# Kernel tuning notes

Measured on AMD Instinct MI355X. Metric: run time of the kernel, lower is better.

The kernel has to match this reference:

```python
import jax, jax.numpy as jnp
import numpy as np

N_NODES = 100000
N_EDGES = 1600000


def _glorot(key, shape):
    lim = float(np.sqrt(6.0 / (shape[0] + shape[1])))
    return jax.random.uniform(key, shape, jnp.float32, -lim, lim)


def setup_inputs() -> dict:
    key = jax.random.key(0)
    ks = jax.random.split(key, 12)
    x = jax.random.normal(ks[0], (N_NODES, 8), jnp.float32)
    edge_index = jax.random.randint(ks[1], (2, N_EDGES), 0, N_NODES, jnp.int64)
    dims = [(8, 32), (32, 32), (32, 32), (32, 32), (32, 3)]
    params = {}
    for i, (din, dout) in enumerate(dims):
        params[f"W{i+1}"] = _glorot(ks[2 + i], (din, dout))
        params[f"b{i+1}"] = jnp.zeros((dout,), jnp.float32)
    return {"x": x, "edge_index": edge_index, **params}


def _gcn_norm(edge_index, num_nodes):
    # add self-loops, symmetric normalization (PyG GCNConv defaults)
    loops = jnp.arange(num_nodes, dtype=edge_index.dtype)
    row = jnp.concatenate([edge_index[0], loops])
    col = jnp.concatenate([edge_index[1], loops])
    deg = jax.ops.segment_sum(jnp.ones_like(col, jnp.float32), col,
                              num_segments=num_nodes)
    dinv = jnp.where(deg > 0, jax.lax.rsqrt(deg), 0.0)
    norm = dinv[row] * dinv[col]  # [E + N]
    return row, col, norm


def _gcn_conv(h, W, b, row, col, norm, num_nodes):
    h = h @ W                                   # [N, dout]
    msg = h[row] * norm[:, None]                # gather + scale
    out = jax.ops.segment_sum(msg, col, num_segments=num_nodes)
    return out + b


def reference(x, edge_index, W1, b1, W2, b2, W3, b3, W4, b4, W5, b5):
    row, col, norm = _gcn_norm(edge_index, N_NODES)
    lrelu = lambda h: jax.nn.leaky_relu(h, negative_slope=1.0)  # identity, kept faithful
    h = lrelu(_gcn_conv(x, W1, b1, row, col, norm, N_NODES))
    h = lrelu(_gcn_conv(h, W2, b2, row, col, norm, N_NODES))
    h = lrelu(_gcn_conv(h, W3, b3, row, col, norm, N_NODES))
    h = lrelu(_gcn_conv(h, W4, b4, row, col, norm, N_NODES))
    h = lrelu(_gcn_conv(h, W5, b5, row, col, norm, N_NODES))
    return h
```

## Files before the change

### kernel.cpp

```cpp
#include <hip/hip_runtime.h>
#include <hip/hip_bf16.h>

#define NN 100000
#define NE 1600000
#define NB 391
#define EPB 3125
#define NBLK 512
#define CAP 4608



__global__ __launch_bounds__(256) void prep_kernel(
    const unsigned int* __restrict__ ew, int* __restrict__ is64,
    const float* __restrict__ W1, const float* __restrict__ b1,
    const float* __restrict__ W2, const float* __restrict__ b2,
    const float* __restrict__ W3, const float* __restrict__ b3,
    const float* __restrict__ W4, const float* __restrict__ b4,
    const float* __restrict__ W5, const float* __restrict__ b5,
    float* __restrict__ Wt, float* __restrict__ cv,
    int* __restrict__ bcursor) {
    __shared__ int nz;
    __shared__ float w45[32 * 3], w345[32 * 3], w2345[32 * 3];
    int tid = threadIdx.x;
    if (tid == 0) nz = 0;
    __syncthreads();
    if (ew[2 * tid + 1] != 0) atomicAdd(&nz, 1);
    for (int i = tid; i < NB; i += 256) bcursor[i] = i * CAP;
    int i = tid / 3, j = tid - 3 * (tid / 3);
    if (tid < 96) {
        float s = 0.0f;
        for (int k = 0; k < 32; k++) s += W4[i * 32 + k] * W5[k * 3 + j];
        w45[i * 3 + j] = s;
    }
    __syncthreads();
    if (tid < 96) {
        float s = 0.0f;
        for (int k = 0; k < 32; k++) s += W3[i * 32 + k] * w45[k * 3 + j];
        w345[i * 3 + j] = s;
    }
    __syncthreads();
    if (tid < 96) {
        float s = 0.0f;
        for (int k = 0; k < 32; k++) s += W2[i * 32 + k] * w345[k * 3 + j];
        w2345[i * 3 + j] = s;
    }
    __syncthreads();
    if (tid < 32) {
        int ii = tid >> 2, jj = tid & 3;
        float s = 0.0f;
        if (jj < 3)
            for (int k = 0; k < 32; k++) s += W1[ii * 32 + k] * w2345[k * 3 + jj];
        Wt[tid] = s;
    }
    if (tid >= 32 && tid < 52) {
        int kk = (tid - 32) >> 2, jj = (tid - 32) & 3;
        float s = 0.0f;
        if (jj < 3) {
            if (kk == 0) for (int k = 0; k < 32; k++) s += b1[k] * w2345[k * 3 + jj];
            if (kk == 1) for (int k = 0; k < 32; k++) s += b2[k] * w345[k * 3 + jj];
            if (kk == 2) for (int k = 0; k < 32; k++) s += b3[k] * w45[k * 3 + jj];
            if (kk == 3) for (int k = 0; k < 32; k++) s += b4[k] * W5[k * 3 + jj];
            if (kk == 4) s = b5[jj];
        }
        cv[tid - 32] = s;
    }
    if (tid == 0) *is64 = (nz == 0) ? 1 : 0;
}


__global__ __launch_bounds__(512) void bucket_scatter_kernel(const void* __restrict__ ei,
                                                             const int* __restrict__ is64,
                                                             int* __restrict__ bcursor,
                                                             unsigned int* __restrict__ epacked) {
    __shared__ int lcount[NB];
    __shared__ int lstart[NB];
    __shared__ int lcur[NB];
    __shared__ int gbase[NB];
    __shared__ int wsum[8];
    __shared__ unsigned int slotv[EPB];
    __shared__ unsigned short slotb[EPB];
    int tid = threadIdx.x;
    for (int i = tid; i < NB; i += 512) lcount[i] = 0;
    __syncthreads();
    int f = *is64;
    int base = blockIdx.x * EPB;
    int r[7], c[7];
    r[6] = -1;
    if (f == 0) {
        const int* e32 = (const int*)ei;
#pragma unroll
        for (int k = 0; k < 6; k++) {
            int e = base + k * 512 + tid;
            r[k] = e32[e];
            c[k] = e32[NE + e];
        }
        if (tid < EPB - 6 * 512) {
            int e = base + 6 * 512 + tid;
            r[6] = e32[e];
            c[6] = e32[NE + e];
        }
    } else {
        const long long* e64 = (const long long*)ei;
#pragma unroll
        for (int k = 0; k < 6; k++) {
            int e = base + k * 512 + tid;
            r[k] = (int)e64[e];
            c[k] = (int)e64[(long long)NE + e];
        }
        if (tid < EPB - 6 * 512) {
            int e = base + 6 * 512 + tid;
            r[6] = (int)e64[e];
            c[6] = (int)e64[(long long)NE + e];
        }
    }
#pragma unroll
    for (int k = 0; k < 7; k++)
        if (r[k] >= 0) atomicAdd(&lcount[c[k] >> 8], 1);
    __syncthreads();
    int lane = tid & 63, w = tid >> 6;
    int v = (tid < NB) ? lcount[tid] : 0;
    int acc = v;
#pragma unroll
    for (int off = 1; off < 64; off <<= 1) {
        int y = __shfl_up(acc, off);
        if (lane >= off) acc += y;
    }
    if (lane == 63) wsum[w] = acc;
    __syncthreads();
    if (tid == 0) {
        int s = 0;
#pragma unroll
        for (int j = 0; j < 8; j++) { int t = wsum[j]; wsum[j] = s; s += t; }
    }
    __syncthreads();
    acc += wsum[w];
    if (tid < NB) {
        int excl = acc - v;
        lstart[tid] = excl;
        lcur[tid] = excl;
    }
    for (int i = tid; i < NB; i += 512) {
        int cnt = lcount[i];
        gbase[i] = cnt ? atomicAdd(&bcursor[i], cnt) : 0;
    }
    __syncthreads();
#pragma unroll
    for (int k = 0; k < 7; k++) {
        if (r[k] >= 0) {
            int b = c[k] >> 8;
            int pos = atomicAdd(&lcur[b], 1);
            slotv[pos] = ((unsigned)(c[k] & 255) << 24) | (unsigned)r[k];
            slotb[pos] = (unsigned short)b;
        }
    }
    __syncthreads();
    for (int s2 = tid; s2 < EPB; s2 += 512) {
        int b = slotb[s2];
        int dst = gbase[b] + (s2 - lstart[b]);
        if (dst < (b + 1) * CAP) epacked[dst] = slotv[s2];
    }
}


__global__ __launch_bounds__(512) void bucket_csr_kernel(const unsigned int* __restrict__ epacked,
                                                         const int* __restrict__ bcursor,
                                                         const float* __restrict__ x,
                                                         const float* __restrict__ Wt,
                                                         int2* __restrict__ meta,
                                                         int* __restrict__ srow,
                                                         float4* __restrict__ Ta, int N) {
    __shared__ int lcount[256];
    __shared__ int lcur[256];
    __shared__ int wsum[4];
    __shared__ float4 Wl[8];
    __shared__ int sbuf[CAP];
    int b = blockIdx.x;
    int tid = threadIdx.x;
    if (tid < 8) Wl[tid] = ((const float4*)Wt)[tid];
    int s0 = b * CAP;
    int cnt = bcursor[b] - s0;
    if (cnt > CAP) cnt = CAP;
    if (tid < 256) lcount[tid] = 0;
    __syncthreads();
    for (int i = tid; i < cnt; i += 512) {
        unsigned int v = epacked[s0 + i];
        atomicAdd(&lcount[v >> 24], 1);
    }
    __syncthreads();
    int lane = tid & 63, w = tid >> 6;
    int myc = (tid < 256) ? lcount[tid] : 0;
    int acc = myc;
#pragma unroll
    for (int off = 1; off < 64; off <<= 1) {
        int y = __shfl_up(acc, off);
        if (lane >= off) acc += y;
    }
    if (lane == 63 && w < 4) wsum[w] = acc;
    __syncthreads();
    if (tid == 0) {
        int s = 0;
#pragma unroll
        for (int j = 0; j < 4; j++) { int t = wsum[j]; wsum[j] = s; s += t; }
    }
    __syncthreads();
    if (tid < 256) {
        int excl = acc - myc + wsum[w];
        lcur[tid] = excl;
        int col = (b << 8) + tid;
        if (col < N) {
            meta[col] = make_int2(s0 + excl, myc);
            float d = 1.0f / sqrtf((float)myc + 1.0f);
            const float4* x4 = (const float4*)x + col * 2;
            float4 av = x4[0], bv = x4[1];
            float xs[8] = {av.x, av.y, av.z, av.w, bv.x, bv.y, bv.z, bv.w};
            float4 o = make_float4(0.f, 0.f, 0.f, 0.f);
#pragma unroll
            for (int k = 0; k < 8; k++) {
                float4 ww = Wl[k];
                o.x += xs[k] * ww.x; o.y += xs[k] * ww.y; o.z += xs[k] * ww.z;
            }
            o.x *= d; o.y *= d; o.z *= d; o.w = 0.0f;
            Ta[col] = o;
        }
    }
    __syncthreads();
    for (int i = tid; i < cnt; i += 512) {
        unsigned int v = epacked[s0 + i];
        int p = atomicAdd(&lcur[v >> 24], 1);
        sbuf[p] = (int)(v & 0xFFFFFFu);
    }
    __syncthreads();
    for (int i = tid; i < cnt; i += 512) srow[s0 + i] = sbuf[i];
}


template <bool LAST>
__global__ __launch_bounds__(256) void prop_kernel(
    const int2* __restrict__ meta, const int* __restrict__ srow,
    const float4* __restrict__ tin, const float* __restrict__ cv, int k,
    float4* __restrict__ tout, float* __restrict__ out, int N) {
    int tid = blockIdx.x * 256 + threadIdx.x;
    int c = tid >> 2, q = tid & 3;
    if (c >= N) return;
    int2 m = meta[c];
    int s = m.x;
    int d = m.y;
    float4 a = (q == 0) ? tin[c] : make_float4(0.f, 0.f, 0.f, 0.f);
    float4 a2 = make_float4(0.f, 0.f, 0.f, 0.f);
    int i = q;
    for (; i + 4 < d; i += 8) {
        int r0 = srow[s + i];
        int r1 = srow[s + i + 4];
        float4 v0 = tin[r0];
        float4 v1 = tin[r1];
        a.x += v0.x; a.y += v0.y; a.z += v0.z;
        a2.x += v1.x; a2.y += v1.y; a2.z += v1.z;
    }
    if (i < d) {
        float4 v = tin[srow[s + i]];
        a.x += v.x; a.y += v.y; a.z += v.z;
    }
    a.x += a2.x; a.y += a2.y; a.z += a2.z;
    a.x += __shfl_xor(a.x, 1); a.y += __shfl_xor(a.y, 1); a.z += __shfl_xor(a.z, 1);
    a.x += __shfl_xor(a.x, 2); a.y += __shfl_xor(a.y, 2); a.z += __shfl_xor(a.z, 2);
    if (q == 0) {
        float dd = 1.0f / sqrtf((float)d + 1.0f);
        float cx = cv[k * 4 + 0], cy = cv[k * 4 + 1], cz = cv[k * 4 + 2];
        if (LAST) {
            out[c * 3 + 0] = dd * a.x + cx;
            out[c * 3 + 1] = dd * a.y + cy;
            out[c * 3 + 2] = dd * a.z + cz;
        } else {
            float d2 = dd * dd;
            float4 o;
            o.x = d2 * a.x + dd * cx;
            o.y = d2 * a.y + dd * cy;
            o.z = d2 * a.z + dd * cz;
            o.w = 0.0f;
            tout[c] = o;
        }
    }
}


extern "C" void kernel_launch(void* const* d_in, const int* in_sizes, int n_in,
                              void* d_out, int out_size, void* d_ws, size_t ws_size,
                              hipStream_t stream) {
    const float* x  = (const float*)d_in[0];
    const void*  ei = d_in[1];
    const float* W1 = (const float*)d_in[2];  const float* b1 = (const float*)d_in[3];
    const float* W2 = (const float*)d_in[4];  const float* b2 = (const float*)d_in[5];
    const float* W3 = (const float*)d_in[6];  const float* b3 = (const float*)d_in[7];
    const float* W4 = (const float*)d_in[8];  const float* b4 = (const float*)d_in[9];
    const float* W5 = (const float*)d_in[10]; const float* b5 = (const float*)d_in[11];
    float* out = (float*)d_out;

    char* p = (char*)d_ws;
    auto alloc = [&](size_t bytes) {
        char* r = p;
        p += (bytes + 255) & ~(size_t)255;
        return r;
    };
    int2*  meta    = (int2*)alloc((size_t)NN * 8);
    int*   is64    = (int*)alloc(256);
    int*   bcursor = (int*)alloc(NB * 4);
    float* Wt      = (float*)alloc(8 * 4 * 4);
    float* cv      = (float*)alloc(5 * 4 * 4);
    unsigned int* epacked = (unsigned int*)alloc((size_t)NB * CAP * 4);
    int*          srow    = (int*)alloc((size_t)NB * CAP * 4);
    float4*       Ta      = (float4*)alloc((size_t)NN * 16);
    float4*       Tb      = (float4*)alloc((size_t)NN * 16);
    if ((size_t)(p - (char*)d_ws) > ws_size) return;

    int gP = (NN * 4 + 255) / 256;
    prep_kernel<<<1, 256, 0, stream>>>((const unsigned int*)ei, is64,
                                       W1, b1, W2, b2, W3, b3, W4, b4, W5, b5,
                                       Wt, cv, bcursor);
    bucket_scatter_kernel<<<NBLK, 512, 0, stream>>>(ei, is64, bcursor, epacked);
    bucket_csr_kernel<<<NB, 512, 0, stream>>>(epacked, bcursor, x, Wt,
                                              meta, srow, Ta, NN);

    prop_kernel<false><<<gP, 256, 0, stream>>>(meta, srow, Ta, cv, 0, Tb, nullptr, NN);
    prop_kernel<false><<<gP, 256, 0, stream>>>(meta, srow, Tb, cv, 1, Ta, nullptr, NN);
    prop_kernel<false><<<gP, 256, 0, stream>>>(meta, srow, Ta, cv, 2, Tb, nullptr, NN);
    prop_kernel<false><<<gP, 256, 0, stream>>>(meta, srow, Tb, cv, 3, Ta, nullptr, NN);
    prop_kernel<true><<<gP, 256, 0, stream>>>(meta, srow, Ta, cv, 4, nullptr, out, NN);
}
```

Baseline: 168.9 us.

## Replace CSR build with bucketed edges and LDS atomic accumulation in propagation

```diff
diff --git a/kernel.cpp b/kernel.cpp
--- a/kernel.cpp
+++ b/kernel.cpp
@@ -162,54 +162,30 @@
 }
 
 
-__global__ __launch_bounds__(512) void bucket_csr_kernel(const unsigned int* __restrict__ epacked,
-                                                         const int* __restrict__ bcursor,
-                                                         const float* __restrict__ x,
-                                                         const float* __restrict__ Wt,
-                                                         int2* __restrict__ meta,
-                                                         int* __restrict__ srow,
-                                                         float4* __restrict__ Ta, int N) {
+__global__ __launch_bounds__(512) void deg_z_kernel(const unsigned int* __restrict__ epacked,
+                                                    const int* __restrict__ bcursor,
+                                                    const float* __restrict__ x,
+                                                    const float* __restrict__ Wt,
+                                                    float* __restrict__ dinv,
+                                                    float4* __restrict__ Ta, int N) {
     __shared__ int lcount[256];
-    __shared__ int lcur[256];
-    __shared__ int wsum[4];
     __shared__ float4 Wl[8];
-    __shared__ int sbuf[CAP];
     int b = blockIdx.x;
     int tid = threadIdx.x;
     if (tid < 8) Wl[tid] = ((const float4*)Wt)[tid];
+    if (tid < 256) lcount[tid] = 0;
     int s0 = b * CAP;
     int cnt = bcursor[b] - s0;
     if (cnt > CAP) cnt = CAP;
-    if (tid < 256) lcount[tid] = 0;
-    __syncthreads();
-    for (int i = tid; i < cnt; i += 512) {
-        unsigned int v = epacked[s0 + i];
-        atomicAdd(&lcount[v >> 24], 1);
-    }
-    __syncthreads();
-    int lane = tid & 63, w = tid >> 6;
-    int myc = (tid < 256) ? lcount[tid] : 0;
-    int acc = myc;
-#pragma unroll
-    for (int off = 1; off < 64; off <<= 1) {
-        int y = __shfl_up(acc, off);
-        if (lane >= off) acc += y;
-    }
-    if (lane == 63 && w < 4) wsum[w] = acc;
-    __syncthreads();
-    if (tid == 0) {
-        int s = 0;
-#pragma unroll
-        for (int j = 0; j < 4; j++) { int t = wsum[j]; wsum[j] = s; s += t; }
-    }
+    __syncthreads();
+    for (int i = tid; i < cnt; i += 512)
+        atomicAdd(&lcount[epacked[s0 + i] >> 24], 1);
     __syncthreads();
     if (tid < 256) {
-        int excl = acc - myc + wsum[w];
-        lcur[tid] = excl;
         int col = (b << 8) + tid;
         if (col < N) {
-            meta[col] = make_int2(s0 + excl, myc);
-            float d = 1.0f / sqrtf((float)myc + 1.0f);
+            float d = 1.0f / sqrtf((float)lcount[tid] + 1.0f);
+            dinv[col] = d;
             const float4* x4 = (const float4*)x + col * 2;
             float4 av = x4[0], bv = x4[1];
             float xs[8] = {av.x, av.y, av.z, av.w, bv.x, bv.y, bv.z, bv.w};
@@ -223,61 +199,64 @@
             Ta[col] = o;
         }
     }
-    __syncthreads();
-    for (int i = tid; i < cnt; i += 512) {
-        unsigned int v = epacked[s0 + i];
-        int p = atomicAdd(&lcur[v >> 24], 1);
-        sbuf[p] = (int)(v & 0xFFFFFFu);
-    }
-    __syncthreads();
-    for (int i = tid; i < cnt; i += 512) srow[s0 + i] = sbuf[i];
 }
 
 
 template <bool LAST>
-__global__ __launch_bounds__(256) void prop_kernel(
-    const int2* __restrict__ meta, const int* __restrict__ srow,
-    const float4* __restrict__ tin, const float* __restrict__ cv, int k,
+__global__ __launch_bounds__(512) void prop_kernel(
+    const unsigned int* __restrict__ epacked, const int* __restrict__ bcursor,
+    const float* __restrict__ dinv, const float4* __restrict__ tin,
+    const float* __restrict__ cv, int kk,
     float4* __restrict__ tout, float* __restrict__ out, int N) {
-    int tid = blockIdx.x * 256 + threadIdx.x;
-    int c = tid >> 2, q = tid & 3;
-    if (c >= N) return;
-    int2 m = meta[c];
-    int s = m.x;
-    int d = m.y;
-    float4 a = (q == 0) ? tin[c] : make_float4(0.f, 0.f, 0.f, 0.f);
-    float4 a2 = make_float4(0.f, 0.f, 0.f, 0.f);
-    int i = q;
-    for (; i + 4 < d; i += 8) {
-        int r0 = srow[s + i];
-        int r1 = srow[s + i + 4];
-        float4 v0 = tin[r0];
-        float4 v1 = tin[r1];
-        a.x += v0.x; a.y += v0.y; a.z += v0.z;
-        a2.x += v1.x; a2.y += v1.y; a2.z += v1.z;
-    }
-    if (i < d) {
-        float4 v = tin[srow[s + i]];
-        a.x += v.x; a.y += v.y; a.z += v.z;
-    }
-    a.x += a2.x; a.y += a2.y; a.z += a2.z;
-    a.x += __shfl_xor(a.x, 1); a.y += __shfl_xor(a.y, 1); a.z += __shfl_xor(a.z, 1);
-    a.x += __shfl_xor(a.x, 2); a.y += __shfl_xor(a.y, 2); a.z += __shfl_xor(a.z, 2);
-    if (q == 0) {
-        float dd = 1.0f / sqrtf((float)d + 1.0f);
-        float cx = cv[k * 4 + 0], cy = cv[k * 4 + 1], cz = cv[k * 4 + 2];
-        if (LAST) {
-            out[c * 3 + 0] = dd * a.x + cx;
-            out[c * 3 + 1] = dd * a.y + cy;
-            out[c * 3 + 2] = dd * a.z + cz;
-        } else {
-            float d2 = dd * dd;
-            float4 o;
-            o.x = d2 * a.x + dd * cx;
-            o.y = d2 * a.y + dd * cy;
-            o.z = d2 * a.z + dd * cz;
-            o.w = 0.0f;
-            tout[c] = o;
+    __shared__ float acc[768];
+    int b = blockIdx.x;
+    int tid = threadIdx.x;
+    for (int i = tid; i < 768; i += 512) acc[i] = 0.0f;
+    int s0 = b * CAP;
+    int cnt = bcursor[b] - s0;
+    if (cnt > CAP) cnt = CAP;
+    __syncthreads();
+    if (cnt > 0) {
+        int last = s0 + cnt - 1;
+        unsigned int ev[9];
+        float4 vv[9];
+#pragma unroll
+        for (int k = 0; k < 9; k++) {
+            int i = s0 + k * 512 + tid;
+            ev[k] = epacked[i < last ? i : last];
+        }
+#pragma unroll
+        for (int k = 0; k < 9; k++)
+            vv[k] = tin[ev[k] & 0xFFFFFFu];
+#pragma unroll
+        for (int k = 0; k < 9; k++) {
+            if (k * 512 + tid < cnt) {
+                int c3 = (int)(ev[k] >> 24) * 3;
+                atomicAdd(&acc[c3 + 0], vv[k].x);
+                atomicAdd(&acc[c3 + 1], vv[k].y);
+                atomicAdd(&acc[c3 + 2], vv[k].z);
+            }
+        }
+    }
+    __syncthreads();
+    if (tid < 256) {
+        int col = (b << 8) + tid;
+        if (col < N) {
+            float4 t = tin[col];
+            float ax = acc[tid * 3 + 0] + t.x;
+            float ay = acc[tid * 3 + 1] + t.y;
+            float az = acc[tid * 3 + 2] + t.z;
+            float dd = dinv[col];
+            float cx = cv[kk * 4 + 0], cy = cv[kk * 4 + 1], cz = cv[kk * 4 + 2];
+            if (LAST) {
+                out[col * 3 + 0] = dd * ax + cx;
+                out[col * 3 + 1] = dd * ay + cy;
+                out[col * 3 + 2] = dd * az + cz;
+            } else {
+                float d2 = dd * dd;
+                tout[col] = make_float4(d2 * ax + dd * cx, d2 * ay + dd * cy,
+                                        d2 * az + dd * cz, 0.0f);
+            }
         }
     }
 }
@@ -301,28 +280,25 @@
         p += (bytes + 255) & ~(size_t)255;
         return r;
     };
-    int2*  meta    = (int2*)alloc((size_t)NN * 8);
+    float* dinv    = (float*)alloc((size_t)NN * 4);
     int*   is64    = (int*)alloc(256);
     int*   bcursor = (int*)alloc(NB * 4);
     float* Wt      = (float*)alloc(8 * 4 * 4);
     float* cv      = (float*)alloc(5 * 4 * 4);
     unsigned int* epacked = (unsigned int*)alloc((size_t)NB * CAP * 4);
-    int*          srow    = (int*)alloc((size_t)NB * CAP * 4);
     float4*       Ta      = (float4*)alloc((size_t)NN * 16);
     float4*       Tb      = (float4*)alloc((size_t)NN * 16);
     if ((size_t)(p - (char*)d_ws) > ws_size) return;
 
-    int gP = (NN * 4 + 255) / 256;
     prep_kernel<<<1, 256, 0, stream>>>((const unsigned int*)ei, is64,
                                        W1, b1, W2, b2, W3, b3, W4, b4, W5, b5,
                                        Wt, cv, bcursor);
     bucket_scatter_kernel<<<NBLK, 512, 0, stream>>>(ei, is64, bcursor, epacked);
-    bucket_csr_kernel<<<NB, 512, 0, stream>>>(epacked, bcursor, x, Wt,
-                                              meta, srow, Ta, NN);
-
-    prop_kernel<false><<<gP, 256, 0, stream>>>(meta, srow, Ta, cv, 0, Tb, nullptr, NN);
-    prop_kernel<false><<<gP, 256, 0, stream>>>(meta, srow, Tb, cv, 1, Ta, nullptr, NN);
-    prop_kernel<false><<<gP, 256, 0, stream>>>(meta, srow, Ta, cv, 2, Tb, nullptr, NN);
-    prop_kernel<false><<<gP, 256, 0, stream>>>(meta, srow, Tb, cv, 3, Ta, nullptr, NN);
-    prop_kernel<true><<<gP, 256, 0, stream>>>(meta, srow, Ta, cv, 4, nullptr, out, NN);
-}
+    deg_z_kernel<<<NB, 512, 0, stream>>>(epacked, bcursor, x, Wt, dinv, Ta, NN);
+
+    prop_kernel<false><<<NB, 512, 0, stream>>>(epacked, bcursor, dinv, Ta, cv, 0, Tb, nullptr, NN);
+    prop_kernel<false><<<NB, 512, 0, stream>>>(epacked, bcursor, dinv, Tb, cv, 1, Ta, nullptr, NN);
+    prop_kernel<false><<<NB, 512, 0, stream>>>(epacked, bcursor, dinv, Ta, cv, 2, Tb, nullptr, NN);
+    prop_kernel<false><<<NB, 512, 0, stream>>>(epacked, bcursor, dinv, Tb, cv, 3, Ta, nullptr, NN);
+    prop_kernel<true><<<NB, 512, 0, stream>>>(epacked, bcursor, dinv, Ta, cv, 4, nullptr, out, NN);
+}
```

New measurement: 301.8 us. +78.6%, slower.

## Fold prep kernel into scatter and CSR kernels, scatter edges directly

Applied to the files above, without the earlier changes.

```diff
diff --git a/kernel.cpp b/kernel.cpp
--- a/kernel.cpp
+++ b/kernel.cpp
@@ -1,5 +1,4 @@
 #include <hip/hip_runtime.h>
-#include <hip/hip_bf16.h>
 
 #define NN 100000
 #define NE 1600000
@@ -10,39 +9,113 @@
 
 
 
-__global__ __launch_bounds__(256) void prep_kernel(
-    const unsigned int* __restrict__ ew, int* __restrict__ is64,
+__global__ __launch_bounds__(512) void bucket_scatter_kernel(const void* __restrict__ ei,
+                                                             int* __restrict__ bcursor,
+                                                             unsigned int* __restrict__ epacked) {
+    __shared__ int lcount[NB];
+    __shared__ int lcur[NB];
+    int tid = threadIdx.x;
+    for (int i = tid; i < NB; i += 512) lcount[i] = 0;
+    int base = blockIdx.x * EPB;
+    unsigned int hw = ((const unsigned int*)ei)[2 * (base + tid) + 1];
+    int is64 = (__ballot(hw != 0) == 0ULL);
+    int r[7], c[7];
+    r[6] = -1;
+    if (!is64) {
+        const int* e32 = (const int*)ei;
+#pragma unroll
+        for (int k = 0; k < 6; k++) {
+            int e = base + k * 512 + tid;
+            r[k] = e32[e];
+            c[k] = e32[NE + e];
+        }
+        if (tid < EPB - 6 * 512) {
+            int e = base + 6 * 512 + tid;
+            r[6] = e32[e];
+            c[6] = e32[NE + e];
+        }
+    } else {
+        const long long* e64 = (const long long*)ei;
+#pragma unroll
+        for (int k = 0; k < 6; k++) {
+            int e = base + k * 512 + tid;
+            r[k] = (int)e64[e];
+            c[k] = (int)e64[(long long)NE + e];
+        }
+        if (tid < EPB - 6 * 512) {
+            int e = base + 6 * 512 + tid;
+            r[6] = (int)e64[e];
+            c[6] = (int)e64[(long long)NE + e];
+        }
+    }
+    __syncthreads();
+#pragma unroll
+    for (int k = 0; k < 7; k++)
+        if (r[k] >= 0) atomicAdd(&lcount[c[k] >> 8], 1);
+    __syncthreads();
+    for (int i = tid; i < NB; i += 512) {
+        int cnt = lcount[i];
+        lcur[i] = (cnt ? atomicAdd(&bcursor[i], cnt) : 0) + i * CAP;
+    }
+    __syncthreads();
+#pragma unroll
+    for (int k = 0; k < 7; k++) {
+        if (r[k] >= 0) {
+            int b = c[k] >> 8;
+            int pos = atomicAdd(&lcur[b], 1);
+            if (pos < (b + 1) * CAP)
+                epacked[pos] = ((unsigned)(c[k] & 255) << 24) | (unsigned)r[k];
+        }
+    }
+}
+
+
+__global__ __launch_bounds__(512) void bucket_csr_kernel(
+    const unsigned int* __restrict__ epacked, const int* __restrict__ bcount,
+    const float* __restrict__ x,
     const float* __restrict__ W1, const float* __restrict__ b1,
     const float* __restrict__ W2, const float* __restrict__ b2,
     const float* __restrict__ W3, const float* __restrict__ b3,
     const float* __restrict__ W4, const float* __restrict__ b4,
     const float* __restrict__ W5, const float* __restrict__ b5,
-    float* __restrict__ Wt, float* __restrict__ cv,
-    int* __restrict__ bcursor) {
-    __shared__ int nz;
-    __shared__ float w45[32 * 3], w345[32 * 3], w2345[32 * 3];
+    float* __restrict__ cv,
+    int2* __restrict__ meta, int* __restrict__ srow,
+    float4* __restrict__ Ta, int N) {
+    __shared__ float w45[96], w345[96], w2345[96];
+    __shared__ float4 Wl4[8];
+    __shared__ int lcount[256];
+    __shared__ int lcur[256];
+    __shared__ int wsum[4];
+    __shared__ int sbuf[CAP];
+    int b = blockIdx.x;
     int tid = threadIdx.x;
-    if (tid == 0) nz = 0;
-    __syncthreads();
-    if (ew[2 * tid + 1] != 0) atomicAdd(&nz, 1);
-    for (int i = tid; i < NB; i += 256) bcursor[i] = i * CAP;
-    int i = tid / 3, j = tid - 3 * (tid / 3);
+    int s0 = b * CAP;
+    int cnt = bcount[b];
+    if (cnt > CAP) cnt = CAP;
+    if (tid < 256) lcount[tid] = 0;
+    int i3 = tid / 3, j3 = tid - 3 * (tid / 3);
     if (tid < 96) {
         float s = 0.0f;
-        for (int k = 0; k < 32; k++) s += W4[i * 32 + k] * W5[k * 3 + j];
-        w45[i * 3 + j] = s;
-    }
-    __syncthreads();
+        for (int k = 0; k < 32; k++) s += W4[i3 * 32 + k] * W5[k * 3 + j3];
+        w45[i3 * 3 + j3] = s;
+    }
+    __syncthreads();
+    unsigned int ev[9];
+#pragma unroll
+    for (int k = 0; k < 9; k++) {
+        int i = k * 512 + tid;
+        ev[k] = (i < cnt) ? epacked[s0 + i] : 0xFFFFFFFFu;
+    }
     if (tid < 96) {
         float s = 0.0f;
-        for (int k = 0; k < 32; k++) s += W3[i * 32 + k] * w45[k * 3 + j];
-        w345[i * 3 + j] = s;
+        for (int k = 0; k < 32; k++) s += W3[i3 * 32 + k] * w45[k * 3 + j3];
+        w345[i3 * 3 + j3] = s;
     }
     __syncthreads();
     if (tid < 96) {
         float s = 0.0f;
-        for (int k = 0; k < 32; k++) s += W2[i * 32 + k] * w345[k * 3 + j];
-        w2345[i * 3 + j] = s;
+        for (int k = 0; k < 32; k++) s += W2[i3 * 32 + k] * w345[k * 3 + j3];
+        w2345[i3 * 3 + j3] = s;
     }
     __syncthreads();
     if (tid < 32) {
@@ -50,9 +123,9 @@
         float s = 0.0f;
         if (jj < 3)
             for (int k = 0; k < 32; k++) s += W1[ii * 32 + k] * w2345[k * 3 + jj];
-        Wt[tid] = s;
-    }
-    if (tid >= 32 && tid < 52) {
+        ((float*)Wl4)[tid] = s;
+    }
+    if (b == 0 && tid >= 32 && tid < 52) {
         int kk = (tid - 32) >> 2, jj = (tid - 32) & 3;
         float s = 0.0f;
         if (jj < 3) {
@@ -64,128 +137,9 @@
         }
         cv[tid - 32] = s;
     }
-    if (tid == 0) *is64 = (nz == 0) ? 1 : 0;
-}
-
-
-__global__ __launch_bounds__(512) void bucket_scatter_kernel(const void* __restrict__ ei,
-                                                             const int* __restrict__ is64,
-                                                             int* __restrict__ bcursor,
-                                                             unsigned int* __restrict__ epacked) {
-    __shared__ int lcount[NB];
-    __shared__ int lstart[NB];
-    __shared__ int lcur[NB];
-    __shared__ int gbase[NB];
-    __shared__ int wsum[8];
-    __shared__ unsigned int slotv[EPB];
-    __shared__ unsigned short slotb[EPB];
-    int tid = threadIdx.x;
-    for (int i = tid; i < NB; i += 512) lcount[i] = 0;
-    __syncthreads();
-    int f = *is64;
-    int base = blockIdx.x * EPB;
-    int r[7], c[7];
-    r[6] = -1;
-    if (f == 0) {
-        const int* e32 = (const int*)ei;
-#pragma unroll
-        for (int k = 0; k < 6; k++) {
-            int e = base + k * 512 + tid;
-            r[k] = e32[e];
-            c[k] = e32[NE + e];
-        }
-        if (tid < EPB - 6 * 512) {
-            int e = base + 6 * 512 + tid;
-            r[6] = e32[e];
-            c[6] = e32[NE + e];
-        }
-    } else {
-        const long long* e64 = (const long long*)ei;
-#pragma unroll
-        for (int k = 0; k < 6; k++) {
-            int e = base + k * 512 + tid;
-            r[k] = (int)e64[e];
-            c[k] = (int)e64[(long long)NE + e];
-        }
-        if (tid < EPB - 6 * 512) {
-            int e = base + 6 * 512 + tid;
-            r[6] = (int)e64[e];
-            c[6] = (int)e64[(long long)NE + e];
-        }
-    }
-#pragma unroll
-    for (int k = 0; k < 7; k++)
-        if (r[k] >= 0) atomicAdd(&lcount[c[k] >> 8], 1);
-    __syncthreads();
-    int lane = tid & 63, w = tid >> 6;
-    int v = (tid < NB) ? lcount[tid] : 0;
-    int acc = v;
-#pragma unroll
-    for (int off = 1; off < 64; off <<= 1) {
-        int y = __shfl_up(acc, off);
-        if (lane >= off) acc += y;
-    }
-    if (lane == 63) wsum[w] = acc;
-    __syncthreads();
-    if (tid == 0) {
-        int s = 0;
-#pragma unroll
-        for (int j = 0; j < 8; j++) { int t = wsum[j]; wsum[j] = s; s += t; }
-    }
-    __syncthreads();
-    acc += wsum[w];
-    if (tid < NB) {
-        int excl = acc - v;
-        lstart[tid] = excl;
-        lcur[tid] = excl;
-    }
-    for (int i = tid; i < NB; i += 512) {
-        int cnt = lcount[i];
-        gbase[i] = cnt ? atomicAdd(&bcursor[i], cnt) : 0;
-    }
-    __syncthreads();
-#pragma unroll
-    for (int k = 0; k < 7; k++) {
-        if (r[k] >= 0) {
-            int b = c[k] >> 8;
-            int pos = atomicAdd(&lcur[b], 1);
-            slotv[pos] = ((unsigned)(c[k] & 255) << 24) | (unsigned)r[k];
-            slotb[pos] = (unsigned short)b;
-        }
-    }
-    __syncthreads();
-    for (int s2 = tid; s2 < EPB; s2 += 512) {
-        int b = slotb[s2];
-        int dst = gbase[b] + (s2 - lstart[b]);
-        if (dst < (b + 1) * CAP) epacked[dst] = slotv[s2];
-    }
-}
-
-
-__global__ __launch_bounds__(512) void bucket_csr_kernel(const unsigned int* __restrict__ epacked,
-                                                         const int* __restrict__ bcursor,
-                                                         const float* __restrict__ x,
-                                                         const float* __restrict__ Wt,
-                                                         int2* __restrict__ meta,
-                                                         int* __restrict__ srow,
-                                                         float4* __restrict__ Ta, int N) {
-    __shared__ int lcount[256];
-    __shared__ int lcur[256];
-    __shared__ int wsum[4];
-    __shared__ float4 Wl[8];
-    __shared__ int sbuf[CAP];
-    int b = blockIdx.x;
-    int tid = threadIdx.x;
-    if (tid < 8) Wl[tid] = ((const float4*)Wt)[tid];
-    int s0 = b * CAP;
-    int cnt = bcursor[b] - s0;
-    if (cnt > CAP) cnt = CAP;
-    if (tid < 256) lcount[tid] = 0;
-    __syncthreads();
-    for (int i = tid; i < cnt; i += 512) {
-        unsigned int v = epacked[s0 + i];
-        atomicAdd(&lcount[v >> 24], 1);
-    }
+#pragma unroll
+    for (int k = 0; k < 9; k++)
+        if (ev[k] != 0xFFFFFFFFu) atomicAdd(&lcount[ev[k] >> 24], 1);
     __syncthreads();
     int lane = tid & 63, w = tid >> 6;
     int myc = (tid < 256) ? lcount[tid] : 0;
@@ -216,7 +170,7 @@
             float4 o = make_float4(0.f, 0.f, 0.f, 0.f);
 #pragma unroll
             for (int k = 0; k < 8; k++) {
-                float4 ww = Wl[k];
+                float4 ww = Wl4[k];
                 o.x += xs[k] * ww.x; o.y += xs[k] * ww.y; o.z += xs[k] * ww.z;
             }
             o.x *= d; o.y *= d; o.z *= d; o.w = 0.0f;
@@ -224,10 +178,12 @@
         }
     }
     __syncthreads();
-    for (int i = tid; i < cnt; i += 512) {
-        unsigned int v = epacked[s0 + i];
-        int p = atomicAdd(&lcur[v >> 24], 1);
-        sbuf[p] = (int)(v & 0xFFFFFFu);
+#pragma unroll
+    for (int k = 0; k < 9; k++) {
+        if (ev[k] != 0xFFFFFFFFu) {
+            int p = atomicAdd(&lcur[ev[k] >> 24], 1);
+            sbuf[p] = (int)(ev[k] & 0xFFFFFFu);
+        }
     }
     __syncthreads();
     for (int i = tid; i < cnt; i += 512) srow[s0 + i] = sbuf[i];
@@ -302,9 +258,7 @@
         return r;
     };
     int2*  meta    = (int2*)alloc((size_t)NN * 8);
-    int*   is64    = (int*)alloc(256);
     int*   bcursor = (int*)alloc(NB * 4);
-    float* Wt      = (float*)alloc(8 * 4 * 4);
     float* cv      = (float*)alloc(5 * 4 * 4);
     unsigned int* epacked = (unsigned int*)alloc((size_t)NB * CAP * 4);
     int*          srow    = (int*)alloc((size_t)NB * CAP * 4);
@@ -312,14 +266,13 @@
     float4*       Tb      = (float4*)alloc((size_t)NN * 16);
     if ((size_t)(p - (char*)d_ws) > ws_size) return;
 
+    hipMemsetAsync(bcursor, 0, NB * 4, stream);
+    bucket_scatter_kernel<<<NBLK, 512, 0, stream>>>(ei, bcursor, epacked);
+    bucket_csr_kernel<<<NB, 512, 0, stream>>>(epacked, bcursor, x,
+                                              W1, b1, W2, b2, W3, b3, W4, b4, W5, b5,
+                                              cv, meta, srow, Ta, NN);
+
     int gP = (NN * 4 + 255) / 256;
-    prep_kernel<<<1, 256, 0, stream>>>((const unsigned int*)ei, is64,
-                                       W1, b1, W2, b2, W3, b3, W4, b4, W5, b5,
-                                       Wt, cv, bcursor);
-    bucket_scatter_kernel<<<NBLK, 512, 0, stream>>>(ei, is64, bcursor, epacked);
-    bucket_csr_kernel<<<NB, 512, 0, stream>>>(epacked, bcursor, x, Wt,
-                                              meta, srow, Ta, NN);
-
     prop_kernel<false><<<gP, 256, 0, stream>>>(meta, srow, Ta, cv, 0, Tb, nullptr, NN);
     prop_kernel<false><<<gP, 256, 0, stream>>>(meta, srow, Tb, cv, 1, Ta, nullptr, NN);
     prop_kernel<false><<<gP, 256, 0, stream>>>(meta, srow, Ta, cv, 2, Tb, nullptr, NN);
```

Result: slower. 173.3 us (+2.6%).
